# Kernel tuning notes

Measured on AMD Instinct MI355X. Metric: run time of the kernel, lower is better.

Reference implementation:

```python
import jax, jax.numpy as jnp
import numpy as np

N_NODES = 100000
N_EDGES = 3200000
IN_F = 500
HID = 64
OUT_F = 64
ALPHA = 0.1
K = 10


def setup_inputs() -> dict:
    key = jax.random.key(0)
    ks = jax.random.split(key, 8)
    x = jax.random.normal(ks[0], (N_NODES, IN_F), dtype=jnp.float32)
    edge_src = jax.random.randint(ks[1], (N_EDGES,), 0, N_NODES, dtype=jnp.int32)
    edge_dst = jax.random.randint(ks[2], (N_EDGES,), 0, N_NODES, dtype=jnp.int32)
    edge_weight = jax.random.uniform(ks[3], (N_EDGES,), dtype=jnp.float32)
    W1 = jax.random.normal(ks[4], (IN_F, HID), dtype=jnp.float32) * (1.0 / np.sqrt(IN_F))
    b1 = jnp.zeros((HID,), dtype=jnp.float32)
    W2 = jax.random.normal(ks[5], (HID, OUT_F), dtype=jnp.float32) * (1.0 / np.sqrt(HID))
    b2 = jnp.zeros((OUT_F,), dtype=jnp.float32)
    return {"x": x, "edge_src": edge_src, "edge_dst": edge_dst,
            "edge_weight": edge_weight, "W1": W1, "b1": b1, "W2": W2, "b2": b2}


def _spmm(edge_src, edge_dst, edge_weight, z):
    # sparse adj @ z : gather rows at src, scale by edge weight, scatter-add at dst
    msg = edge_weight[:, None] * z[edge_src]          # [E, C]
    return jax.ops.segment_sum(msg, edge_dst, num_segments=N_NODES)


def reference(x, edge_src, edge_dst, edge_weight, W1, b1, W2, b2):
    # MLP encoder (dropout is identity at inference)
    h = jax.nn.relu(x @ W1 + b1) @ W2 + b2            # [N, OUT_F]
    # APPNP propagation: z_{k+1} = (1-alpha) * A z_k + alpha * h
    z = h
    for _ in range(K):
        z = (1.0 - ALPHA) * _spmm(edge_src, edge_dst, edge_weight, z) + ALPHA * h
    return z
```

## Files before the change

kernel.cpp:

```cpp
#include <hip/hip_runtime.h>

#define N_NODES 100000
#define N_EDGES 3200000
#define IN_F 500
#define HID 64
#define OUT_F 64
#define ALPHA 0.1f
#define K_ITERS 10
#define SCAN_B ((N_NODES + 255) / 256)

#define NPART 8
#define PART_N (N_NODES / NPART)
#define FILL_GRID 2048

typedef unsigned short ushort_t;
typedef unsigned int uint_t;
typedef int iv4 __attribute__((ext_vector_type(4)));

__device__ __forceinline__ float bf2f(ushort_t v) {
    union { uint_t u; float f; } c; c.u = ((uint_t)v) << 16; return c.f;
}
__device__ __forceinline__ ushort_t f2b(float f) {
    union { float f; uint_t u; } c; c.f = f;
    uint_t u = c.u + 0x7fffu + ((c.u >> 16) & 1u);
    return (ushort_t)(u >> 16);
}
__device__ __forceinline__ float bflo(uint_t u) {
    union { uint_t u; float f; } c; c.u = u << 16; return c.f;
}
__device__ __forceinline__ float bfhi(uint_t u) {
    union { uint_t u; float f; } c; c.u = u & 0xffff0000u; return c.f;
}
__device__ __forceinline__ uint_t packbf(float a, float b) {
    return (uint_t)f2b(a) | ((uint_t)f2b(b) << 16);
}

__global__ __launch_bounds__(256) void mlp_kernel(
    const float* __restrict__ x, const float* __restrict__ W1,
    const float* __restrict__ b1, const float* __restrict__ W2,
    const float* __restrict__ b2, ushort_t* __restrict__ hb,
    ushort_t* __restrict__ ahb)
{
    __shared__ float xs[32][100];
    __shared__ float hid[32][64];

    const int tid = threadIdx.x;
    const int c   = tid & 63;
    const int rg  = tid >> 6;
    const int block_row = blockIdx.x * 32;

    float acc[8] = {0.f, 0.f, 0.f, 0.f, 0.f, 0.f, 0.f, 0.f};

    for (int kb = 0; kb < IN_F; kb += 100) {
        for (int i = tid; i < 800; i += 256) {
            int r = i / 25, c4 = i - r * 25;
            *(float4*)&xs[r][c4 * 4] =
                *(const float4*)&x[(long)(block_row + r) * IN_F + kb + c4 * 4];
        }
        __syncthreads();
        for (int k = 0; k < 100; k += 4) {
            float w0 = W1[(kb+k+0)*HID + c];
            float w1 = W1[(kb+k+1)*HID + c];
            float w2 = W1[(kb+k+2)*HID + c];
            float w3 = W1[(kb+k+3)*HID + c];
            #pragma unroll
            for (int r = 0; r < 8; ++r) {
                float4 xv = *(const float4*)&xs[rg*8+r][k];
                acc[r] = fmaf(xv.x, w0, acc[r]);
                acc[r] = fmaf(xv.y, w1, acc[r]);
                acc[r] = fmaf(xv.z, w2, acc[r]);
                acc[r] = fmaf(xv.w, w3, acc[r]);
            }
        }
        __syncthreads();
    }

    float b = b1[c];
    #pragma unroll
    for (int r = 0; r < 8; ++r)
        hid[rg*8+r][c] = fmaxf(acc[r] + b, 0.f);
    __syncthreads();

    float o[8] = {0.f, 0.f, 0.f, 0.f, 0.f, 0.f, 0.f, 0.f};
    for (int k = 0; k < HID; k += 4) {
        float w0 = W2[(k+0)*OUT_F + c], w1 = W2[(k+1)*OUT_F + c];
        float w2 = W2[(k+2)*OUT_F + c], w3 = W2[(k+3)*OUT_F + c];
        #pragma unroll
        for (int r = 0; r < 8; ++r) {
            float4 hv = *(const float4*)&hid[rg*8+r][k];
            o[r] = fmaf(hv.x, w0, o[r]);
            o[r] = fmaf(hv.y, w1, o[r]);
            o[r] = fmaf(hv.z, w2, o[r]);
            o[r] = fmaf(hv.w, w3, o[r]);
        }
    }
    float bb = b2[c];
    int r0 = block_row + rg * 8;
    #pragma unroll
    for (int r = 0; r < 8; ++r) {
        float v = o[r] + bb;
        hb[(r0+r)*64 + c]  = f2b(v);
        ahb[(r0+r)*64 + c] = f2b(ALPHA * v);
    }
}

__global__ __launch_bounds__(256) void zero_cnt(int* __restrict__ cnt)
{
    int i = blockIdx.x * 256 + threadIdx.x;
    if (i < N_NODES) cnt[i] = 0;
}

__global__ __launch_bounds__(256) void count_keys(
    const int* __restrict__ key, int* __restrict__ cnt)
{
    int i = blockIdx.x * 256 + threadIdx.x;
    if (i < N_EDGES) atomicAdd(&cnt[key[i]], 1);
}

__global__ __launch_bounds__(256) void scan_block_sums(
    const int* __restrict__ cnt, int* __restrict__ bsum)
{
    int i = blockIdx.x * 256 + threadIdx.x;
    int v = (i < N_NODES) ? cnt[i] : 0;
    for (int off = 32; off; off >>= 1) v += __shfl_down(v, off);
    __shared__ int ws_[4];
    if ((threadIdx.x & 63) == 0) ws_[threadIdx.x >> 6] = v;
    __syncthreads();
    if (threadIdx.x == 0) bsum[blockIdx.x] = ws_[0] + ws_[1] + ws_[2] + ws_[3];
}

__global__ __launch_bounds__(512) void scan_partials(
    const int* __restrict__ bsum, int* __restrict__ boff)
{
    int t = threadIdx.x;
    int v = (t < SCAN_B) ? bsum[t] : 0;
    int lane = t & 63, w = t >> 6;
    int x = v;
    for (int off = 1; off < 64; off <<= 1) {
        int y = __shfl_up(x, off);
        if (lane >= off) x += y;
    }
    __shared__ int wsum[8];
    if (lane == 63) wsum[w] = x;
    __syncthreads();
    if (w == 0) {
        int s = (lane < 8) ? wsum[lane] : 0;
        for (int off = 1; off < 8; off <<= 1) {
            int y = __shfl_up(s, off);
            if (lane >= off) s += y;
        }
        if (lane < 8) wsum[lane] = s;
    }
    __syncthreads();
    int wpre = (w == 0) ? 0 : wsum[w - 1];
    if (t < SCAN_B) boff[t] = wpre + x - v;
}

__global__ __launch_bounds__(256) void scan_final(
    const int* __restrict__ cnt, const int* __restrict__ boff,
    int* __restrict__ row_start, int* __restrict__ pos)
{
    int i = blockIdx.x * 256 + threadIdx.x;
    int v = (i < N_NODES) ? cnt[i] : 0;
    int lane = threadIdx.x & 63, w = threadIdx.x >> 6;
    int x = v;
    for (int off = 1; off < 64; off <<= 1) {
        int y = __shfl_up(x, off);
        if (lane >= off) x += y;
    }
    __shared__ int wsum[4];
    if (lane == 63) wsum[w] = x;
    __syncthreads();
    int wpre = 0;
    for (int ww = 0; ww < w; ++ww) wpre += wsum[ww];
    int excl = wpre + x - v;
    int r = boff[blockIdx.x] + excl;
    if (i < N_NODES) { row_start[i] = r; pos[i] = r; }
    if (i == 0) row_start[N_NODES] = N_EDGES;
}

__global__ __launch_bounds__(256) void fill_dst_part(
    const int* __restrict__ esrc, const int* __restrict__ edst,
    const float* __restrict__ ew, int* __restrict__ pos,
    int2* __restrict__ csr)
{
    const int part = blockIdx.x & (NPART - 1);
    const int lo = part * PART_N;
    const int hi = lo + PART_N;
    const int pthreads = (FILL_GRID / NPART) * 256;
    const int NQUAD = N_EDGES / 4;

    for (int qd = (blockIdx.x >> 3) * 256 + threadIdx.x; qd < NQUAD; qd += pthreads) {
        iv4 d4 = __builtin_nontemporal_load((const iv4*)edst + qd);
        const int i0 = qd * 4;
#define DO_EDGE(DV, IDX) do {                                        \
        int d_ = (DV);                                               \
        if (d_ >= lo && d_ < hi) {                                   \
            int   s_ = __builtin_nontemporal_load(&esrc[IDX]);       \
            float w_ = __builtin_nontemporal_load(&ew[IDX]);         \
            int   q_ = atomicAdd(&pos[d_], 1);                       \
            csr[q_] = make_int2(s_, __float_as_int(0.9f * w_));      \
        } } while (0)
        DO_EDGE(d4.x, i0 + 0);
        DO_EDGE(d4.y, i0 + 1);
        DO_EDGE(d4.z, i0 + 2);
        DO_EDGE(d4.w, i0 + 3);
#undef DO_EDGE
    }
}

__global__ __launch_bounds__(256) void sort_rows(
    const int* __restrict__ row_start, int2* __restrict__ csr)
{
    const int node = blockIdx.x * 4 + (threadIdx.x >> 6);
    const int lane = threadIdx.x & 63;
    const int s0 = row_start[node];
    const int s1 = row_start[node + 1];
    int n = s1 - s0; if (n > 64) n = 64;
    int key = 0x7fffffff;
    int val = 0;
    if (lane < n) { int2 e = csr[s0 + lane]; key = e.x; val = e.y; }
    #pragma unroll
    for (int k = 2; k <= 64; k <<= 1) {
        #pragma unroll
        for (int j = k >> 1; j > 0; j >>= 1) {
            int pk = __shfl_xor(key, j, 64);
            int pv = __shfl_xor(val, j, 64);
            bool lower   = (lane & j) == 0;
            bool asc     = (lane & k) == 0;
            bool takeMin = (lower == asc);
            bool pick    = takeMin ? (pk < key) : (pk > key);
            if (pick) { key = pk; val = pv; }
        }
    }
    if (lane < n) csr[s0 + lane] = make_int2(key, val);
}

template <bool FINAL>
__global__ __launch_bounds__(256) void spmm_kernel(
    const int* __restrict__ row_start, const int2* __restrict__ csr,
    const ushort_t* __restrict__ zin, const ushort_t* __restrict__ ahb,
    void* __restrict__ zout)
{
    const int node = blockIdx.x * 4 + (threadIdx.x >> 6);
    const int lane = threadIdx.x & 63;
    const int g = lane >> 3;
    const int q = lane & 7;
    const int s0 = __builtin_amdgcn_readfirstlane(row_start[node]);
    const int s1 = __builtin_amdgcn_readfirstlane(row_start[node + 1]);

    float a0=0.f,a1=0.f,a2=0.f,a3=0.f,a4=0.f,a5=0.f,a6=0.f,a7=0.f;
    if (g == 0) {
        uint4 t = *(const uint4*)&ahb[node * 64 + 8 * q];
        a0 = bflo(t.x); a1 = bfhi(t.x); a2 = bflo(t.y); a3 = bfhi(t.y);
        a4 = bflo(t.z); a5 = bfhi(t.z); a6 = bflo(t.w); a7 = bfhi(t.w);
    }

#define FMA8(WV, ZV) do { \
        a0 = fmaf((WV), bflo((ZV).x), a0); a1 = fmaf((WV), bfhi((ZV).x), a1); \
        a2 = fmaf((WV), bflo((ZV).y), a2); a3 = fmaf((WV), bfhi((ZV).y), a3); \
        a4 = fmaf((WV), bflo((ZV).z), a4); a5 = fmaf((WV), bfhi((ZV).z), a5); \
        a6 = fmaf((WV), bflo((ZV).w), a6); a7 = fmaf((WV), bfhi((ZV).w), a7); \
    } while (0)

    int j = s0;
    for (; j + 32 <= s1; j += 32) {
        int2 e0 = csr[j + g];
        int2 e1 = csr[j + 8 + g];
        int2 e2 = csr[j + 16 + g];
        int2 e3 = csr[j + 24 + g];
        uint4 z0 = *(const uint4*)&zin[e0.x * 64 + 8 * q];
        uint4 z1 = *(const uint4*)&zin[e1.x * 64 + 8 * q];
        uint4 z2 = *(const uint4*)&zin[e2.x * 64 + 8 * q];
        uint4 z3 = *(const uint4*)&zin[e3.x * 64 + 8 * q];
        float w0 = __int_as_float(e0.y);
        float w1 = __int_as_float(e1.y);
        float w2 = __int_as_float(e2.y);
        float w3 = __int_as_float(e3.y);
        FMA8(w0, z0);
        FMA8(w1, z1);
        FMA8(w2, z2);
        FMA8(w3, z3);
    }
    for (; j < s1; j += 8) {
        int2 e = make_int2(0, 0);
        int jj = j + g;
        if (jj < s1) e = csr[jj];
        uint4 zt = *(const uint4*)&zin[e.x * 64 + 8 * q];
        float wt = __int_as_float(e.y);
        FMA8(wt, zt);
    }
#undef FMA8

    #pragma unroll
    for (int m = 8; m <= 32; m <<= 1) {
        a0 += __shfl_xor(a0, m, 64); a1 += __shfl_xor(a1, m, 64);
        a2 += __shfl_xor(a2, m, 64); a3 += __shfl_xor(a3, m, 64);
        a4 += __shfl_xor(a4, m, 64); a5 += __shfl_xor(a5, m, 64);
        a6 += __shfl_xor(a6, m, 64); a7 += __shfl_xor(a7, m, 64);
    }

    if (g == 0) {
        if (FINAL) {
            float* op = (float*)zout + node * 64 + 8 * q;
            *(float4*)op       = make_float4(a0, a1, a2, a3);
            *(float4*)(op + 4) = make_float4(a4, a5, a6, a7);
        } else {
            uint4 pk;
            pk.x = packbf(a0, a1); pk.y = packbf(a2, a3);
            pk.z = packbf(a4, a5); pk.w = packbf(a6, a7);
            *(uint4*)&((ushort_t*)zout)[node * 64 + 8 * q] = pk;
        }
    }
}

extern "C" void kernel_launch(void* const* d_in, const int* in_sizes, int n_in,
                              void* d_out, int out_size, void* d_ws, size_t ws_size,
                              hipStream_t stream)
{
    const float* x    = (const float*)d_in[0];
    const int*   esrc = (const int*)d_in[1];
    const int*   edst = (const int*)d_in[2];
    const float* ew   = (const float*)d_in[3];
    const float* W1   = (const float*)d_in[4];
    const float* b1   = (const float*)d_in[5];
    const float* W2   = (const float*)d_in[6];
    const float* b2   = (const float*)d_in[7];
    float* out = (float*)d_out;

    char* p = (char*)d_ws;
    ushort_t* ahb = (ushort_t*)p;  p += (size_t)N_NODES * 64 * 2;
    ushort_t* hb  = (ushort_t*)p;  p += (size_t)N_NODES * 64 * 2;
    ushort_t* zB  = (ushort_t*)p;  p += (size_t)N_NODES * 64 * 2;
    int2*  csr     = (int2*)p;     p += (size_t)N_EDGES * 8;
    int* cnt       = (int*)p;      p += (size_t)N_NODES * 4;
    int* pos       = (int*)p;      p += (size_t)N_NODES * 4;
    int* row_start = (int*)p;      p += (size_t)(N_NODES + 1) * 4;
    int* bsum      = (int*)p;      p += (size_t)SCAN_B * 4;
    int* boff      = (int*)p;      p += (size_t)SCAN_B * 4;

    const int EB = (N_EDGES + 255) / 256;

    hipLaunchKernelGGL(mlp_kernel, dim3(N_NODES / 32), dim3(256), 0, stream,
                       x, W1, b1, W2, b2, hb, ahb);

    hipLaunchKernelGGL(zero_cnt, dim3(SCAN_B), dim3(256), 0, stream, cnt);
    hipLaunchKernelGGL(count_keys, dim3(EB), dim3(256), 0, stream, edst, cnt);
    hipLaunchKernelGGL(scan_block_sums, dim3(SCAN_B), dim3(256), 0, stream, cnt, bsum);
    hipLaunchKernelGGL(scan_partials, dim3(1), dim3(512), 0, stream, bsum, boff);
    hipLaunchKernelGGL(scan_final, dim3(SCAN_B), dim3(256), 0, stream,
                       cnt, boff, row_start, pos);
    hipLaunchKernelGGL(fill_dst_part, dim3(FILL_GRID), dim3(256), 0, stream,
                       esrc, edst, ew, pos, csr);
    hipLaunchKernelGGL(sort_rows, dim3(N_NODES / 4), dim3(256), 0, stream,
                       row_start, csr);

    const ushort_t* zi = hb;
    for (int it = 0; it < K_ITERS - 1; ++it) {
        ushort_t* zo = (it % 2 == 0) ? zB : hb;
        hipLaunchKernelGGL((spmm_kernel<false>), dim3(N_NODES / 4), dim3(256), 0, stream,
                           row_start, csr, zi, ahb, (void*)zo);
        zi = zo;
    }
    hipLaunchKernelGGL((spmm_kernel<true>), dim3(N_NODES / 4), dim3(256), 0, stream,
                       row_start, csr, zi, ahb, (void*)out);
}
```

Baseline: 1.395 ms.

## Compute MLP encoder with bf16 MFMA instead of scalar FMA

```diff
diff --git a/kernel.cpp b/kernel.cpp
--- a/kernel.cpp
+++ b/kernel.cpp
@@ -13,9 +13,13 @@
 #define PART_N (N_NODES / NPART)
 #define FILL_GRID 2048
 
+#define KPAD 512
+
 typedef unsigned short ushort_t;
 typedef unsigned int uint_t;
 typedef int iv4 __attribute__((ext_vector_type(4)));
+typedef __attribute__((ext_vector_type(8))) short bf16x8;
+typedef __attribute__((ext_vector_type(4))) float f32x4;
 
 __device__ __forceinline__ float bf2f(ushort_t v) {
     union { uint_t u; float f; } c; c.u = ((uint_t)v) << 16; return c.f;
@@ -34,73 +38,113 @@
 __device__ __forceinline__ uint_t packbf(float a, float b) {
     return (uint_t)f2b(a) | ((uint_t)f2b(b) << 16);
 }
-
-__global__ __launch_bounds__(256) void mlp_kernel(
-    const float* __restrict__ x, const float* __restrict__ W1,
-    const float* __restrict__ b1, const float* __restrict__ W2,
+__device__ __forceinline__ bf16x8 pack8(float4 a, float4 b) {
+    bf16x8 r;
+    r[0] = (short)f2b(a.x); r[1] = (short)f2b(a.y);
+    r[2] = (short)f2b(a.z); r[3] = (short)f2b(a.w);
+    r[4] = (short)f2b(b.x); r[5] = (short)f2b(b.y);
+    r[6] = (short)f2b(b.z); r[7] = (short)f2b(b.w);
+    return r;
+}
+
+__global__ __launch_bounds__(256) void prep_weights(
+    const float* __restrict__ W1, const float* __restrict__ W2,
+    ushort_t* __restrict__ w1t, ushort_t* __restrict__ w2t)
+{
+    int i = blockIdx.x * 256 + threadIdx.x;
+    if (i < 64 * KPAD) {
+        int c = i >> 9, k = i & (KPAD - 1);
+        float v = (k < IN_F) ? W1[k * HID + c] : 0.f;
+        w1t[c * KPAD + k] = f2b(v);
+    } else {
+        int j = i - 64 * KPAD;
+        if (j < 64 * 64) {
+            int c = j >> 6, k = j & 63;
+            w2t[c * 64 + k] = f2b(W2[k * OUT_F + c]);
+        }
+    }
+}
+
+__global__ __launch_bounds__(256) void mlp_mfma(
+    const float* __restrict__ x, const ushort_t* __restrict__ w1t,
+    const float* __restrict__ b1, const ushort_t* __restrict__ w2t,
     const float* __restrict__ b2, ushort_t* __restrict__ hb,
     ushort_t* __restrict__ ahb)
 {
-    __shared__ float xs[32][100];
-    __shared__ float hid[32][64];
-
-    const int tid = threadIdx.x;
-    const int c   = tid & 63;
-    const int rg  = tid >> 6;
-    const int block_row = blockIdx.x * 32;
-
-    float acc[8] = {0.f, 0.f, 0.f, 0.f, 0.f, 0.f, 0.f, 0.f};
-
-    for (int kb = 0; kb < IN_F; kb += 100) {
-        for (int i = tid; i < 800; i += 256) {
-            int r = i / 25, c4 = i - r * 25;
-            *(float4*)&xs[r][c4 * 4] =
-                *(const float4*)&x[(long)(block_row + r) * IN_F + kb + c4 * 4];
-        }
-        __syncthreads();
-        for (int k = 0; k < 100; k += 4) {
-            float w0 = W1[(kb+k+0)*HID + c];
-            float w1 = W1[(kb+k+1)*HID + c];
-            float w2 = W1[(kb+k+2)*HID + c];
-            float w3 = W1[(kb+k+3)*HID + c];
+    __shared__ ushort_t hs[4][16][64];
+
+    const int lane = threadIdx.x & 63;
+    const int wid  = threadIdx.x >> 6;
+    const int r16  = lane & 15;
+    const int kg   = lane >> 4;
+    const int rowbase = blockIdx.x * 64 + wid * 16;
+
+    int arow  = rowbase + r16;
+    int lrow  = (arow < N_NODES) ? arow : (N_NODES - 1);
+    const float* xr = x + (long)lrow * IN_F;
+
+    f32x4 acc[4];
+    #pragma unroll
+    for (int t = 0; t < 4; ++t) acc[t] = (f32x4){0.f, 0.f, 0.f, 0.f};
+
+    for (int ks = 0; ks < KPAD / 32; ++ks) {
+        const int k0 = ks * 32 + kg * 8;
+        bf16x8 af;
+        if (k0 + 8 <= IN_F) {
+            float4 xa = *(const float4*)(xr + k0);
+            float4 xb = *(const float4*)(xr + k0 + 4);
+            af = pack8(xa, xb);
+        } else {
             #pragma unroll
-            for (int r = 0; r < 8; ++r) {
-                float4 xv = *(const float4*)&xs[rg*8+r][k];
-                acc[r] = fmaf(xv.x, w0, acc[r]);
-                acc[r] = fmaf(xv.y, w1, acc[r]);
-                acc[r] = fmaf(xv.z, w2, acc[r]);
-                acc[r] = fmaf(xv.w, w3, acc[r]);
+            for (int i = 0; i < 8; ++i) {
+                float v = (k0 + i < IN_F) ? xr[k0 + i] : 0.f;
+                af[i] = (short)f2b(v);
             }
         }
-        __syncthreads();
-    }
-
-    float b = b1[c];
-    #pragma unroll
-    for (int r = 0; r < 8; ++r)
-        hid[rg*8+r][c] = fmaxf(acc[r] + b, 0.f);
+        #pragma unroll
+        for (int t = 0; t < 4; ++t) {
+            bf16x8 bfw = *(const bf16x8*)&w1t[(t * 16 + r16) * KPAD + k0];
+            acc[t] = __builtin_amdgcn_mfma_f32_16x16x32_bf16(af, bfw, acc[t], 0, 0, 0);
+        }
+    }
+
+    #pragma unroll
+    for (int t = 0; t < 4; ++t) {
+        float bb = b1[t * 16 + r16];
+        #pragma unroll
+        for (int r = 0; r < 4; ++r) {
+            float h = fmaxf(acc[t][r] + bb, 0.f);
+            hs[wid][kg * 4 + r][t * 16 + r16] = f2b(h);
+        }
+    }
     __syncthreads();
 
-    float o[8] = {0.f, 0.f, 0.f, 0.f, 0.f, 0.f, 0.f, 0.f};
-    for (int k = 0; k < HID; k += 4) {
-        float w0 = W2[(k+0)*OUT_F + c], w1 = W2[(k+1)*OUT_F + c];
-        float w2 = W2[(k+2)*OUT_F + c], w3 = W2[(k+3)*OUT_F + c];
+    f32x4 acc2[4];
+    #pragma unroll
+    for (int t = 0; t < 4; ++t) acc2[t] = (f32x4){0.f, 0.f, 0.f, 0.f};
+
+    #pragma unroll
+    for (int ks = 0; ks < 2; ++ks) {
+        bf16x8 ha = *(const bf16x8*)&hs[wid][r16][ks * 32 + kg * 8];
         #pragma unroll
-        for (int r = 0; r < 8; ++r) {
-            float4 hv = *(const float4*)&hid[rg*8+r][k];
-            o[r] = fmaf(hv.x, w0, o[r]);
-            o[r] = fmaf(hv.y, w1, o[r]);
-            o[r] = fmaf(hv.z, w2, o[r]);
-            o[r] = fmaf(hv.w, w3, o[r]);
-        }
-    }
-    float bb = b2[c];
-    int r0 = block_row + rg * 8;
-    #pragma unroll
-    for (int r = 0; r < 8; ++r) {
-        float v = o[r] + bb;
-        hb[(r0+r)*64 + c]  = f2b(v);
-        ahb[(r0+r)*64 + c] = f2b(ALPHA * v);
+        for (int t = 0; t < 4; ++t) {
+            bf16x8 wb = *(const bf16x8*)&w2t[(t * 16 + r16) * 64 + ks * 32 + kg * 8];
+            acc2[t] = __builtin_amdgcn_mfma_f32_16x16x32_bf16(ha, wb, acc2[t], 0, 0, 0);
+        }
+    }
+
+    #pragma unroll
+    for (int t = 0; t < 4; ++t) {
+        float bb = b2[t * 16 + r16];
+        #pragma unroll
+        for (int r = 0; r < 4; ++r) {
+            int orow = rowbase + kg * 4 + r;
+            if (orow < N_NODES) {
+                float v = acc2[t][r] + bb;
+                hb[orow * 64 + t * 16 + r16]  = f2b(v);
+                ahb[orow * 64 + t * 16 + r16] = f2b(ALPHA * v);
+            }
+        }
     }
 }
 
@@ -338,11 +382,15 @@
     int* row_start = (int*)p;      p += (size_t)(N_NODES + 1) * 4;
     int* bsum      = (int*)p;      p += (size_t)SCAN_B * 4;
     int* boff      = (int*)p;      p += (size_t)SCAN_B * 4;
+    ushort_t* w1t  = (ushort_t*)p; p += (size_t)64 * KPAD * 2;
+    ushort_t* w2t  = (ushort_t*)p; p += (size_t)64 * 64 * 2;
 
     const int EB = (N_EDGES + 255) / 256;
 
-    hipLaunchKernelGGL(mlp_kernel, dim3(N_NODES / 32), dim3(256), 0, stream,
-                       x, W1, b1, W2, b2, hb, ahb);
+    hipLaunchKernelGGL(prep_weights, dim3((64 * KPAD + 64 * 64 + 255) / 256),
+                       dim3(256), 0, stream, W1, W2, w1t, w2t);
+    hipLaunchKernelGGL(mlp_mfma, dim3((N_NODES + 63) / 64), dim3(256), 0, stream,
+                       x, w1t, b1, w2t, b2, hb, ahb);
 
     hipLaunchKernelGGL(zero_cnt, dim3(SCAN_B), dim3(256), 0, stream, cnt);
     hipLaunchKernelGGL(count_keys, dim3(EB), dim3(256), 0, stream, edst, cnt);
```

After: 1.317 ms. 1.06x faster.
